# Kernel tuning notes

Hardware: AMD Instinct MI355X
Metric: run time of the kernel (lower is better)

The kernel has to match this reference:

```python
import jax, jax.numpy as jnp
import numpy as np

BS = 128          # block_size
NB_R, NB_C = 8, 8 # 1024/128 blocks per dim
L = 256           # num_levels = 2**num_bits
T = 100.0         # fixed_T
EPS = 1e-6


def _to_blocks(w):
    # [R, C] -> [num_blocks, BS, BS], row-major block order (matches torch loop i outer, j inner)
    return w.reshape(NB_R, BS, NB_C, BS).transpose(0, 2, 1, 3).reshape(NB_R * NB_C, BS, BS)


def _from_blocks(b):
    return b.reshape(NB_R, NB_C, BS, BS).transpose(0, 2, 1, 3).reshape(NB_R * BS, NB_C * BS)


def setup_inputs() -> dict:
    key = jax.random.key(0)
    weight = jax.random.normal(key, (NB_R * BS, NB_C * BS), dtype=jnp.float32)
    blocks = _to_blocks(weight)
    # per-block min/max parameters, initialized exactly as the torch __init__ does
    w_min = blocks.min(axis=(1, 2))  # [num_blocks]
    w_max = blocks.max(axis=(1, 2))  # [num_blocks]
    return {"weight": weight, "w_min": w_min, "w_max": w_max}


def reference(weight, w_min, w_max):
    blocks = _to_blocks(weight)                                   # [nb, BS, BS]
    # clamp exactly as torch: w_min <= w_max - eps, then w_max >= w_min_clamped + eps
    wmin = jnp.minimum(w_min, w_max - EPS)[:, None, None]         # [nb,1,1]
    wmax = jnp.maximum(w_max[:, None, None], wmin + EPS)          # [nb,1,1]
    scale = wmax - wmin
    w_norm = (blocks - wmin) / (scale + EPS)                      # [nb, BS, BS]

    q_levels = jnp.linspace(0.0, 1.0, L, dtype=jnp.float32)       # [L]
    dists = -jnp.abs(w_norm[..., None] - q_levels)                # [nb, BS, BS, L]
    soft_probs = jax.nn.softmax(dists * T, axis=-1)               # [nb, BS, BS, L]
    w_q = jnp.einsum('nijl,l->nij', soft_probs, q_levels)         # [nb, BS, BS]
    w_deq = w_q * scale + wmin                                    # [nb, BS, BS]

    # entropy: torch sums over dim=0 of each (BS, BS, L) block -> (BS, L) mass
    bin_mass = soft_probs.sum(axis=1)                             # [nb, BS, L]
    bin_probs = bin_mass / (bin_mass.sum(axis=(1, 2), keepdims=True) + EPS)
    total_entropy = -(bin_probs * jnp.log(bin_probs + EPS)).sum()

    dequant = _from_blocks(w_deq)                                 # [1024, 1024]
    return dequant, total_entropy
```

## Files before the change

### kernel.cpp

```cpp
#include <hip/hip_runtime.h>
#include <math.h>


#define NT 512
#define LVL 256
#define PSC 256.0f
#define INV_PSC (1.0f / 256.0f)
#define DEPIDX(c, l) ((((l) & 15) * 272) + ((c) * 17) + ((l) >> 4))
#define NDEP 4352

__global__ __launch_bounds__(NT)
void bq_main(const float* __restrict__ Wt,
             const float* __restrict__ wmin_in,
             const float* __restrict__ wmax_in,
             float* __restrict__ dq_out,
             float* __restrict__ partials)
{
    __shared__ float2 tabK[LVL];
    __shared__ float2 tabJ[LVL];
    __shared__ unsigned dep[NDEP];
    __shared__ float   arrU[NDEP];
    __shared__ float wred[8];

    const int tid = threadIdx.x;
    const int wg  = blockIdx.x;
    const int n = wg >> 3, slab = wg & 7;

    const float LN2 = 0.69314718055994531f;
    const float L2R = -(100.0f / 255.0f) * 1.4426950408889634f;
    const float r = __builtin_amdgcn_exp2f(L2R);
    const float inv1mr = 1.0f / (1.0f - r);

    if (tid < LVL) {
        const int k = tid;
        const float rk1 = __builtin_amdgcn_exp2f(L2R * (float)(k + 1));
        const float A = (1.0f - rk1) * inv1mr;
        const float B = (r - (float)(k + 1) * rk1 + (float)k * rk1 * r)
                        * (inv1mr * inv1mr);
        tabK[k] = make_float2(A, (float)k * A - B);
        tabJ[k] = make_float2(A, (float)(255 - k) * A + B);
    }
    for (int q = tid; q < NDEP; q += NT) dep[q] = 0u;

    const float bmn = wmin_in[n], bmx = wmax_in[n];
    const float wmn = fminf(bmn, bmx - 1e-6f);
    const float wmx = fmaxf(bmx, wmn + 1e-6f);
    const float scale = wmx - wmn;
    const float invsc = 255.0f / (scale + 1e-6f);
    const float sc255 = scale * (1.0f / 255.0f);

    __syncthreads();

    {
        const int row = tid >> 2;
        const int c0  = (tid & 3) * 4;
        const int R = (n >> 3) * 128 + row;
        const int C = (n & 7) * 128 + slab * 16 + c0;
        const float4 x4 = *reinterpret_cast<const float4*>(Wt + (size_t)R * 1024 + C);
        float xs[4] = {x4.x, x4.y, x4.z, x4.w};
        float dq[4];
        #pragma unroll
        for (int u = 0; u < 4; ++u) {
            const float p = (xs[u] - wmn) * invsc;
            int k = (int)p; k = (k > 254) ? 254 : k;
            const float f   = p - (float)k;
            const float rf  = __builtin_amdgcn_exp2f(L2R * f);
            const float r1f = __builtin_amdgcn_exp2f(L2R * (1.0f - f));
            const float2 K = tabK[k];
            const float2 J = tabJ[254 - k];
            const float S  = rf * K.x + r1f * J.x;
            const float Wn = rf * K.y + r1f * J.y;
            const float invS = __builtin_amdgcn_rcpf(S);
            dq[u] = Wn * invS * sc255 + wmn;
            const int c = c0 + u;
            const unsigned dn = (unsigned)(rf  * invS * PSC + 0.5f);
            const unsigned up = (unsigned)(r1f * invS * PSC + 0.5f);
            atomicAdd(&dep[DEPIDX(c, k)], dn | (up << 16));
        }
        float4 o4; o4.x = dq[0]; o4.y = dq[1]; o4.z = dq[2]; o4.w = dq[3];
        *reinterpret_cast<float4*>(dq_out + (size_t)R * 1024 + C) = o4;
    }
    __syncthreads();

    {
        const int ch  = tid & 15;
        const int col = (tid >> 4) & 15;
        const int dir = tid >> 8;
        float lv[16];
        float v = 0.0f;
        if (dir == 0) {
            #pragma unroll
            for (int i = 15; i >= 0; --i) {
                const int l = ch * 16 + i;
                v = v * r + (float)(dep[DEPIDX(col, l)] & 0xffffu) * INV_PSC;
                lv[i] = v;
            }
        } else {
            #pragma unroll
            for (int i = 0; i < 16; ++i) {
                const int l = ch * 16 + i;
                const unsigned w = (l > 0) ? dep[DEPIDX(col, l - 1)] : 0u;
                v = v * r + (float)(w >> 16) * INV_PSC;
                lv[i] = v;
            }
        }
        const float r16 = __builtin_amdgcn_exp2f(L2R * 16.0f);
        float u = v, rp = r16;
        #pragma unroll
        for (int s = 1; s <= 8; s <<= 1) {
            const float o = (dir == 0) ? __shfl_down(u, s, 16) : __shfl_up(u, s, 16);
            const bool ok = (dir == 0) ? (ch + s < 16) : (ch >= s);
            u += ok ? rp * o : 0.0f;
            rp *= rp;
        }
        float cv;
        if (dir == 0) cv = (ch < 15) ? __shfl_down(u, 1, 16) : 0.0f;
        else          cv = (ch > 0)  ? __shfl_up(u, 1, 16)  : 0.0f;

        __syncthreads();

        float* fD = reinterpret_cast<float*>(&dep[0]);
        float m = cv * r;
        if (dir == 0) {
            #pragma unroll
            for (int i = 15; i >= 0; --i) {
                const int l = ch * 16 + i;
                fD[DEPIDX(col, l)] = lv[i] + m; m *= r;
            }
        } else {
            #pragma unroll
            for (int i = 0; i < 16; ++i) {
                const int l = ch * 16 + i;
                arrU[DEPIDX(col, l)] = lv[i] + m; m *= r;
            }
        }
    }
    __syncthreads();

    const float* fD = reinterpret_cast<const float*>(&dep[0]);
    float hsum = 0.0f;
    #pragma unroll
    for (int t = 0; t < 8; ++t) {
        const int q = tid + t * NT;
        const int c = q & 15, l = q >> 4;
        const int idx = DEPIDX(c, l);
        const float b  = fD[idx] + arrU[idx];
        const float ph = b * (1.0f / 16384.0f);
        hsum -= ph * (__builtin_amdgcn_logf(ph + 1e-6f) * LN2);
    }
    #pragma unroll
    for (int off = 32; off > 0; off >>= 1) hsum += __shfl_down(hsum, off);
    if ((tid & 63) == 0) wred[tid >> 6] = hsum;
    __syncthreads();
    if (tid == 0) {
        float tot = 0.0f;
        #pragma unroll
        for (int w = 0; w < 8; ++w) tot += wred[w];
        partials[wg] = tot;
    }
}

__global__ __launch_bounds__(256)
void bq_finish(const float* __restrict__ partials, float* __restrict__ ent_out)
{
    const int tid = threadIdx.x;
    float v = partials[tid] + partials[tid + 256];
    #pragma unroll
    for (int off = 32; off > 0; off >>= 1) v += __shfl_down(v, off);
    __shared__ float buf[4];
    if ((tid & 63) == 0) buf[tid >> 6] = v;
    __syncthreads();
    if (tid == 0) ent_out[0] = buf[0] + buf[1] + buf[2] + buf[3];
}

extern "C" void kernel_launch(void* const* d_in, const int* in_sizes, int n_in,
                              void* d_out, int out_size, void* d_ws, size_t ws_size,
                              hipStream_t stream)
{
    const float* Wt  = (const float*)d_in[0];
    const float* wmn = (const float*)d_in[1];
    const float* wmx = (const float*)d_in[2];
    float* out = (float*)d_out;
    float* partials = (float*)d_ws;

    bq_main<<<512, NT, 0, stream>>>(Wt, wmn, wmx, out, partials);
    bq_finish<<<1, 256, 0, stream>>>(partials, out + 1048576);
}
```

Baseline: 12.44 us.

## Fuse bidirectional scan with entropy in registers, merge level tables, hoist loads

The down and up geometric scans now run in the same thread over 8 levels, using a 32-lane segmented shuffle scan per column. Both directions are combined and fed straight into the entropy log in registers, which removes the arrU shared array, the write-back to LDS and two barriers. The two float2 lookup tables become one float4 table, built with repeated squaring instead of exp2, so each element needs a single LDS read. The global weight and min/max loads are hoisted above table setup so their latency overlaps it. In exchange each thread does more register work, and the scan now runs over 32 lanes instead of 16.

```diff
diff --git a/kernel.cpp b/kernel.cpp
--- a/kernel.cpp
+++ b/kernel.cpp
@@ -16,15 +16,20 @@
              float* __restrict__ dq_out,
              float* __restrict__ partials)
 {
-    __shared__ float2 tabK[LVL];
-    __shared__ float2 tabJ[LVL];
+    __shared__ float4 tab4[LVL];
     __shared__ unsigned dep[NDEP];
-    __shared__ float   arrU[NDEP];
     __shared__ float wred[8];
 
     const int tid = threadIdx.x;
     const int wg  = blockIdx.x;
     const int n = wg >> 3, slab = wg & 7;
+
+    const int row = tid >> 2;
+    const int c0  = (tid & 3) * 4;
+    const int R = (n >> 3) * 128 + row;
+    const int C = (n & 7) * 128 + slab * 16 + c0;
+    const float4 x4 = *reinterpret_cast<const float4*>(Wt + (size_t)R * 1024 + C);
+    const float bmn = wmin_in[n], bmx = wmax_in[n];
 
     const float LN2 = 0.69314718055994531f;
     const float L2R = -(100.0f / 255.0f) * 1.4426950408889634f;
@@ -32,17 +37,27 @@
     const float inv1mr = 1.0f / (1.0f - r);
 
     if (tid < LVL) {
-        const int k = tid;
-        const float rk1 = __builtin_amdgcn_exp2f(L2R * (float)(k + 1));
-        const float A = (1.0f - rk1) * inv1mr;
-        const float B = (r - (float)(k + 1) * rk1 + (float)k * rk1 * r)
-                        * (inv1mr * inv1mr);
-        tabK[k] = make_float2(A, (float)k * A - B);
-        tabJ[k] = make_float2(A, (float)(255 - k) * A + B);
+        float rb[9];
+        rb[0] = r;
+        #pragma unroll
+        for (int b = 1; b < 9; ++b) rb[b] = rb[b - 1] * rb[b - 1];
+        const unsigned e1 = tid + 1;
+        const unsigned e2 = (~tid) & 255u;
+        float rk1 = 1.0f, rj1 = 1.0f;
+        #pragma unroll
+        for (int b = 0; b < 9; ++b) if ((e1 >> b) & 1u) rk1 *= rb[b];
+        #pragma unroll
+        for (int b = 0; b < 8; ++b) if ((e2 >> b) & 1u) rj1 *= rb[b];
+        const float k  = (float)tid;
+        const float Ak = (1.0f - rk1) * inv1mr;
+        const float Bk = (r - (k + 1.0f) * rk1 + k * rk1 * r) * (inv1mr * inv1mr);
+        const float Aj = (1.0f - rj1) * inv1mr;
+        const float Bj = (r - (255.0f - k) * rj1 + (254.0f - k) * rj1 * r)
+                         * (inv1mr * inv1mr);
+        tab4[tid] = make_float4(Ak, k * Ak - Bk, Aj, (k + 1.0f) * Aj + Bj);
     }
     for (int q = tid; q < NDEP; q += NT) dep[q] = 0u;
 
-    const float bmn = wmin_in[n], bmx = wmax_in[n];
     const float wmn = fminf(bmn, bmx - 1e-6f);
     const float wmx = fmaxf(bmx, wmn + 1e-6f);
     const float scale = wmx - wmn;
@@ -52,11 +67,6 @@
     __syncthreads();
 
     {
-        const int row = tid >> 2;
-        const int c0  = (tid & 3) * 4;
-        const int R = (n >> 3) * 128 + row;
-        const int C = (n & 7) * 128 + slab * 16 + c0;
-        const float4 x4 = *reinterpret_cast<const float4*>(Wt + (size_t)R * 1024 + C);
         float xs[4] = {x4.x, x4.y, x4.z, x4.w};
         float dq[4];
         #pragma unroll
@@ -66,87 +76,67 @@
             const float f   = p - (float)k;
             const float rf  = __builtin_amdgcn_exp2f(L2R * f);
             const float r1f = __builtin_amdgcn_exp2f(L2R * (1.0f - f));
-            const float2 K = tabK[k];
-            const float2 J = tabJ[254 - k];
-            const float S  = rf * K.x + r1f * J.x;
-            const float Wn = rf * K.y + r1f * J.y;
+            const float4 t = tab4[k];
+            const float S  = rf * t.x + r1f * t.z;
+            const float Wn = rf * t.y + r1f * t.w;
             const float invS = __builtin_amdgcn_rcpf(S);
             dq[u] = Wn * invS * sc255 + wmn;
-            const int c = c0 + u;
             const unsigned dn = (unsigned)(rf  * invS * PSC + 0.5f);
             const unsigned up = (unsigned)(r1f * invS * PSC + 0.5f);
-            atomicAdd(&dep[DEPIDX(c, k)], dn | (up << 16));
+            atomicAdd(&dep[DEPIDX(c0 + u, k)], dn | (up << 16));
         }
         float4 o4; o4.x = dq[0]; o4.y = dq[1]; o4.z = dq[2]; o4.w = dq[3];
         *reinterpret_cast<float4*>(dq_out + (size_t)R * 1024 + C) = o4;
     }
     __syncthreads();
 
+    float hsum = 0.0f;
     {
-        const int ch  = tid & 15;
-        const int col = (tid >> 4) & 15;
-        const int dir = tid >> 8;
-        float lv[16];
-        float v = 0.0f;
-        if (dir == 0) {
-            #pragma unroll
-            for (int i = 15; i >= 0; --i) {
-                const int l = ch * 16 + i;
-                v = v * r + (float)(dep[DEPIDX(col, l)] & 0xffffu) * INV_PSC;
-                lv[i] = v;
-            }
-        } else {
-            #pragma unroll
-            for (int i = 0; i < 16; ++i) {
-                const int l = ch * 16 + i;
-                const unsigned w = (l > 0) ? dep[DEPIDX(col, l - 1)] : 0u;
-                v = v * r + (float)(w >> 16) * INV_PSC;
-                lv[i] = v;
-            }
+        const int col = tid >> 5;
+        const int ch  = tid & 31;
+        const int l0  = ch * 8;
+        unsigned wd[9];
+        wd[0] = (ch > 0) ? dep[DEPIDX(col, l0 - 1)] : 0u;
+        #pragma unroll
+        for (int j = 0; j < 8; ++j) wd[j + 1] = dep[DEPIDX(col, l0 + j)];
+
+        float lvD[8], lvU[8];
+        float vD = 0.0f;
+        #pragma unroll
+        for (int i = 7; i >= 0; --i) {
+            vD = vD * r + (float)(wd[i + 1] & 0xffffu) * INV_PSC;
+            lvD[i] = vD;
         }
-        const float r16 = __builtin_amdgcn_exp2f(L2R * 16.0f);
-        float u = v, rp = r16;
+        float vU = 0.0f;
         #pragma unroll
-        for (int s = 1; s <= 8; s <<= 1) {
-            const float o = (dir == 0) ? __shfl_down(u, s, 16) : __shfl_up(u, s, 16);
-            const bool ok = (dir == 0) ? (ch + s < 16) : (ch >= s);
-            u += ok ? rp * o : 0.0f;
+        for (int i = 0; i < 8; ++i) {
+            vU = vU * r + (float)(wd[i] >> 16) * INV_PSC;
+            lvU[i] = vU;
+        }
+        float r8 = r * r; r8 = r8 * r8; r8 = r8 * r8;
+        float uD = vD, uU = vU, rp = r8;
+        #pragma unroll
+        for (int s = 1; s <= 16; s <<= 1) {
+            const float oD = __shfl_down(uD, s, 32);
+            const float oU = __shfl_up(uU, s, 32);
+            if (ch + s < 32) uD += rp * oD;
+            if (ch >= s)     uU += rp * oU;
             rp *= rp;
         }
-        float cv;
-        if (dir == 0) cv = (ch < 15) ? __shfl_down(u, 1, 16) : 0.0f;
-        else          cv = (ch > 0)  ? __shfl_up(u, 1, 16)  : 0.0f;
+        const float cvD = (ch < 31) ? __shfl_down(uD, 1, 32) : 0.0f;
+        const float cvU = (ch > 0)  ? __shfl_up(uU, 1, 32)  : 0.0f;
 
-        __syncthreads();
-
-        float* fD = reinterpret_cast<float*>(&dep[0]);
-        float m = cv * r;
-        if (dir == 0) {
-            #pragma unroll
-            for (int i = 15; i >= 0; --i) {
-                const int l = ch * 16 + i;
-                fD[DEPIDX(col, l)] = lv[i] + m; m *= r;
-            }
-        } else {
-            #pragma unroll
-            for (int i = 0; i < 16; ++i) {
-                const int l = ch * 16 + i;
-                arrU[DEPIDX(col, l)] = lv[i] + m; m *= r;
-            }
+        float DD[8];
+        float m = cvD * r;
+        #pragma unroll
+        for (int i = 7; i >= 0; --i) { DD[i] = lvD[i] + m; m *= r; }
+        m = cvU * r;
+        #pragma unroll
+        for (int i = 0; i < 8; ++i) {
+            const float b  = DD[i] + lvU[i] + m; m *= r;
+            const float ph = b * (1.0f / 16384.0f);
+            hsum -= ph * (__builtin_amdgcn_logf(ph + 1e-6f) * LN2);
         }
-    }
-    __syncthreads();
-
-    const float* fD = reinterpret_cast<const float*>(&dep[0]);
-    float hsum = 0.0f;
-    #pragma unroll
-    for (int t = 0; t < 8; ++t) {
-        const int q = tid + t * NT;
-        const int c = q & 15, l = q >> 4;
-        const int idx = DEPIDX(c, l);
-        const float b  = fD[idx] + arrU[idx];
-        const float ph = b * (1.0f / 16384.0f);
-        hsum -= ph * (__builtin_amdgcn_logf(ph + 1e-6f) * LN2);
     }
     #pragma unroll
     for (int off = 32; off > 0; off >>= 1) hsum += __shfl_down(hsum, off);
```

New measurement: 11.79 us. 1.06x faster.
